# Kernel optimization log

Measured on AMD Instinct MI355X. Metric: run time of the kernel, lower is better.

## Reference

```python
import jax, jax.numpy as jnp
import numpy as np

H = 14
N = H * H
DIM = 768
INT = 5
LAM = 3.5


def fft_conv_grouped(x, w):
    # x: (B, g*in_c, N) real; w: (g, int_c, in_c, H, H//2+1) complex
    g, int_c, in_c = w.shape[:3]
    B = x.shape[0]
    xf = jnp.fft.rfftn(x.reshape(B, g, in_c, H, H), axes=(-2, -1), norm='ortho')
    yf = jnp.einsum('bgchf,gichf->bgihf', xf, w)
    y = jnp.fft.irfftn(yf, s=(H, H), axes=(-2, -1), norm='ortho')
    return y.reshape(B, g * int_c, N)


def soft(x, t):
    # sign(x) * relu(|x| - t)
    return jnp.sign(x) * jnp.maximum(jnp.abs(x) - t, 0.0)


def batch_norm(x, gamma, beta, eps=1e-5):
    # training-mode BatchNorm1d applied per channel over (B, N); x: (B, N, C)
    m = x.mean(axis=(0, 1))
    v = x.var(axis=(0, 1))
    return (x - m) * jax.lax.rsqrt(v + eps) * gamma + beta


def setup_inputs() -> dict:
    key = jax.random.key(0)
    ks = jax.random.split(key, 8)
    B = 32
    Hf = H // 2 + 1
    # kernel: init randn*0.06, then normalize_parameters()
    kr = jax.random.normal(ks[0], (DIM, INT, 1, H, Hf, 2), dtype=jnp.float32) * 0.06
    kc = kr[..., 0] + 1j * kr[..., 1]
    nrm = jnp.sqrt((jnp.abs(kc) ** 2).sum(axis=(2, 3, 4), keepdims=True) * 2.0 / H ** 2)
    kc = kc / nrm
    kernel = jnp.stack([jnp.real(kc), jnp.imag(kc)], axis=-1)
    # L buffer: update_L(lam=1) -> per-group max singular value of Gram kk
    kk = jnp.einsum('gichf,gjchf->gijhf', kc, jnp.conj(kc))
    sv = np.linalg.svd(np.asarray(jnp.transpose(kk, (0, 3, 4, 1, 2))), compute_uv=False)
    L = jnp.asarray(sv.reshape(DIM, -1).max(axis=-1), dtype=jnp.float32)
    hid = 4 * DIM
    return {
        'x': jax.random.normal(ks[1], (B, N, DIM), dtype=jnp.float32),
        'v_w': jax.random.normal(ks[2], (DIM, DIM), dtype=jnp.float32) * 0.02,
        'proj_w': jax.random.normal(ks[3], (DIM, DIM), dtype=jnp.float32) * 0.02,
        'proj_b': jnp.zeros((DIM,), dtype=jnp.float32),
        'kernel': kernel,
        'kernel2': jax.random.normal(ks[4], (DIM, 1, 1, H, Hf, 2), dtype=jnp.float32) * 0.02,
        'n1_g': jnp.ones((DIM,), dtype=jnp.float32),
        'n1_b': jnp.zeros((DIM,), dtype=jnp.float32),
        'n2_g': jnp.ones((DIM,), dtype=jnp.float32),
        'n2_b': jnp.zeros((DIM,), dtype=jnp.float32),
        'fc1_w': jax.random.normal(ks[5], (hid, DIM), dtype=jnp.float32) * 0.02,
        'fc1_b': jnp.zeros((hid,), dtype=jnp.float32),
        'fc2_w': jax.random.normal(ks[6], (DIM, hid), dtype=jnp.float32) * 0.02,
        'fc2_b': jnp.zeros((DIM,), dtype=jnp.float32),
        'L': L,
    }


def reference(x, v_w, proj_w, proj_b, kernel, kernel2, n1_g, n1_b, n2_g, n2_b, fc1_w, fc1_b, fc2_w, fc2_b, L):
    k = kernel[..., 0] + 1j * kernel[..., 1]                 # (g, int, 1, H, Hf)
    kk = jnp.einsum('gichf,gjchf->gijhf', k, jnp.conj(k))     # (g, int, int, H, Hf)
    vx = x @ v_w.T                                            # v Linear, no bias
    xc = jnp.swapaxes(vx, -2, -1)                             # (B, C, N)
    u = fft_conv_grouped(xc, k)                               # (B, g*int, N)
    Lv = jnp.repeat(L, INT)[None, :, None]                    # (1, g*int, 1)
    # ISTA: init soft-threshold then 3 gradient + shrink steps
    s = soft(u, LAM)
    for _ in range(3):
        s = s - (fft_conv_grouped(s, kk) - u) / Lv
        s = soft(s, LAM / Lv)
    # reconstruct with conjugate-transposed kernel, then mix with kernel2
    new = fft_conv_grouped(s, jnp.swapaxes(jnp.conj(k), 1, 2))  # (B, g, N)
    k2 = kernel2[..., 0] + 1j * kernel2[..., 1]
    new = fft_conv_grouped(new, k2)
    new = jnp.swapaxes(new, -2, -1)                           # (B, N, C)
    new = x + (batch_norm(new, n1_g, n1_b) @ proj_w.T + proj_b)
    h = jax.nn.gelu(batch_norm(new, n2_g, n2_b) @ fc1_w.T + fc1_b, approximate=False)
    return new + (h @ fc2_w.T + fc2_b)
```

## Files before the change

### kernel.cpp

```cpp
#include <hip/hip_runtime.h>
#include <cmath>

typedef unsigned short u16;
typedef __bf16 bf16x8 __attribute__((ext_vector_type(8)));
typedef float f32x4 __attribute__((ext_vector_type(4)));
typedef float float4v __attribute__((ext_vector_type(4)));
typedef u16 ushort4v __attribute__((ext_vector_type(4)));
typedef u16 ushort8v __attribute__((ext_vector_type(8)));

#define DIMC 768
#define NP 196
#define MTOT 6272
#define HIDC 3072
#define LAMC 3.5f

__device__ const float C14d[14] = {
  1.0f, 0.9009688679024191f, 0.6234898018587336f, 0.22252093395631445f,
  -0.22252093395631445f, -0.6234898018587336f, -0.9009688679024191f, -1.0f,
  -0.9009688679024191f, -0.6234898018587336f, -0.22252093395631445f,
  0.22252093395631445f, 0.6234898018587336f, 0.9009688679024191f
};
__device__ const float S14d[14] = {
  0.0f, 0.43388373911755823f, 0.7818314824680298f, 0.9749279121818236f,
  0.9749279121818236f, 0.7818314824680298f, 0.43388373911755823f, 0.0f,
  -0.43388373911755823f, -0.7818314824680298f, -0.9749279121818236f,
  -0.9749279121818236f, -0.7818314824680298f, -0.43388373911755823f
};

__device__ __forceinline__ u16 f2bf(float f) {
  unsigned u = __builtin_bit_cast(unsigned, f);
  unsigned r = u + 0x7FFFu + ((u >> 16) & 1u);
  return (u16)(r >> 16);
}

__device__ __forceinline__ size_t fidx(int m, int k, int K) {
  return ((size_t)(m >> 4) * (K >> 5) + (k >> 5)) * 512 +
         (size_t)((((k >> 3) & 3) * 16 + (m & 15)) * 8 + (k & 7));
}

__global__ __launch_bounds__(256) void prep_k(
    const float* __restrict__ v_w, const float* __restrict__ fc2w,
    const float* __restrict__ x,
    u16* __restrict__ vwf, u16* __restrict__ fc2f, u16* __restrict__ xf,
    u16* __restrict__ Ff, u16* __restrict__ Gf) {
  const int bid = blockIdx.x, t = threadIdx.x;
  if (bid < 378) {
    int idx = bid * 256 + t;
    if (idx < 50176) {
      int j = idx & 7, lane = (idx >> 3) & 63;
      int mk = idx >> 9, k0 = mk % 7, m0 = mk / 7;
      int s = m0 * 16 + (lane & 15);
      int q = k0 * 32 + (lane >> 4) * 8 + j;
      float v = 0.f;
      if (q < 196) {
        int kr = s >> 4, f = (s >> 1) & 7, r = q / 14, c = q % 14;
        int th = (kr * r + f * c) % 14;
        v = (s & 1) ? -S14d[th] : C14d[th];
      }
      Ff[idx] = f2bf(v);
    } else {
      int t2 = idx - 50176;
      int j = t2 & 7, lane = (t2 >> 3) & 63;
      int pk = t2 >> 9, k0 = pk % 7, p0 = pk / 7;
      int p = p0 * 16 + (lane & 15);
      int s = k0 * 32 + (lane >> 4) * 8 + j;
      float v = 0.f;
      if (p < 196) {
        int kr = s >> 4, f = (s >> 1) & 7, r = p / 14, c = p % 14;
        int th = (kr * r + f * c) % 14;
        float w = (f == 0 || f == 7) ? 1.f : 2.f;
        v = (w * (1.f / 196.f)) * ((s & 1) ? -S14d[th] : C14d[th]);
      }
      Gf[t2] = f2bf(v);
    }
    return;
  }
  const float* src; u16* dst; int idx, K;
  if (bid < 666)        { src = v_w;  dst = vwf;  idx = (bid - 378) * 256 + t;  K = DIMC; }
  else if (bid < 1818)  { src = fc2w; dst = fc2f; idx = (bid - 666) * 256 + t;  K = HIDC; }
  else                  { src = x;    dst = xf;   idx = (bid - 1818) * 256 + t; K = DIMC; }
  const int KC = K >> 5;
  int chunk = idx >> 6, l = idx & 63;
  int row = (chunk / KC) * 16 + (l & 15);
  int k0 = (chunk % KC) * 32 + (l >> 4) * 8;
  const float* sp = src + (size_t)row * K + k0;
  float4v f0 = *(const float4v*)sp;
  float4v f1 = *(const float4v*)(sp + 4);
  ushort8v o;
#pragma unroll
  for (int j = 0; j < 4; ++j) { o[j] = f2bf(f0[j]); o[j + 4] = f2bf(f1[j]); }
  *(ushort8v*)(dst + (size_t)idx * 8) = o;
}

template<int EPI>
__global__ __launch_bounds__(256) void gemmw_k(
    const u16* __restrict__ Af, const u16* __restrict__ Bf,
    const float* __restrict__ bias, const float* __restrict__ res,
    void* __restrict__ Cp, int Nr, int Kr, int NB) {
  const int t = threadIdx.x, w = t >> 6, lane = t & 63;
  const int bid = blockIdx.x;
  const int xcd = bid & 7, j = bid >> 3;
  const int mt = xcd + 8 * (j / NB);
  if (mt >= 98) return;
  const int m0 = mt * 64;
  const int n0 = ((j % NB) * 4 + w) * 64;
  const int KC = Kr >> 5;
  const int l15 = lane & 15, l4 = lane >> 4;

  const u16* Ab = Af + ((size_t)(m0 >> 4) * KC) * 512 + lane * 8;
  const u16* Bb = Bf + ((size_t)(n0 >> 4) * KC) * 512 + lane * 8;

  f32x4 acc[4][4];
#pragma unroll
  for (int a = 0; a < 4; ++a)
#pragma unroll
    for (int b2 = 0; b2 < 4; ++b2) acc[a][b2] = (f32x4){0.f, 0.f, 0.f, 0.f};

  for (int kc = 0; kc < KC; ++kc) {
    bf16x8 af[4], bfv[4];
#pragma unroll
    for (int mb = 0; mb < 4; ++mb)
      af[mb] = *(const bf16x8*)(Ab + ((size_t)mb * KC + kc) * 512);
#pragma unroll
    for (int nb = 0; nb < 4; ++nb)
      bfv[nb] = *(const bf16x8*)(Bb + ((size_t)nb * KC + kc) * 512);
#pragma unroll
    for (int mb = 0; mb < 4; ++mb)
#pragma unroll
      for (int nb = 0; nb < 4; ++nb)
        acc[mb][nb] = __builtin_amdgcn_mfma_f32_16x16x32_bf16(af[mb], bfv[nb], acc[mb][nb], 0, 0, 0);
  }

#pragma unroll
  for (int mb = 0; mb < 4; ++mb) {
#pragma unroll
    for (int nb = 0; nb < 4; ++nb) {
      int n = n0 + nb * 16 + l15;
      if (EPI == 0) {
        int m0r = m0 + mb * 16 + l4 * 4;
        int bb = m0r / 196, np0 = m0r - bb * 196;
        *(float4v*)&((float*)Cp)[((size_t)bb * DIMC + n) * 196 + np0] =
            (float4v){acc[mb][nb][0], acc[mb][nb][1], acc[mb][nb][2], acc[mb][nb][3]};
      } else {
#pragma unroll
        for (int r = 0; r < 4; ++r) {
          int m = m0 + mb * 16 + l4 * 4 + r;
          float v = acc[mb][nb][r];
          if (EPI == 1) {
            ((float*)Cp)[(size_t)m * Nr + n] = v + bias[n] + res[(size_t)m * Nr + n];
          } else {
            float vb = v + bias[n];
            float ge = 0.5f * vb * (1.f + erff(vb * 0.70710678118654752f));
            ((u16*)Cp)[fidx(m, n, Nr)] = f2bf(ge);
          }
        }
      }
    }
  }
}

__global__ __launch_bounds__(64) void checkmfma_k(
    const float* __restrict__ vxt, const float* __restrict__ kern,
    const u16* __restrict__ Ff, const u16* __restrict__ Gf,
    int* __restrict__ cnt, int* __restrict__ wl) {
  __shared__ float xf[16 * 228];
  const int lane = threadIdx.x;
  const int wgb = blockIdx.x;
  const int g = wgb >> 1, bhalf = wgb & 1;
  const int tl = lane & 15, h = lane >> 4;
  const float* xbase = vxt + ((size_t)(bhalf * 16 + tl) * DIMC + g) * 196;

  bf16x8 Bx[7];
#pragma unroll
  for (int k0 = 0; k0 < 7; ++k0) {
    int q0 = k0 * 32 + h * 8;
    ushort8v tv;
    if (k0 < 6) {
      float4v f0 = *(const float4v*)(xbase + q0);
      float4v f1 = *(const float4v*)(xbase + q0 + 4);
#pragma unroll
      for (int j = 0; j < 4; ++j) { tv[j] = f2bf(f0[j]); tv[j + 4] = f2bf(f1[j]); }
    } else {
#pragma unroll
      for (int j = 0; j < 8; ++j) {
        int q = q0 + j;
        tv[j] = (q < 196) ? f2bf(xbase[q]) : (u16)0;
      }
    }
    Bx[k0] = __builtin_bit_cast(bf16x8, tv);
  }

  for (int m0 = 0; m0 < 14; ++m0) {
    f32x4 acc = (f32x4){0.f, 0.f, 0.f, 0.f};
#pragma unroll
    for (int k0 = 0; k0 < 7; ++k0) {
      bf16x8 Af = __builtin_bit_cast(bf16x8,
          *(const ushort8v*)(Ff + ((size_t)(m0 * 7 + k0) * 64 + lane) * 8));
      acc = __builtin_amdgcn_mfma_f32_16x16x32_bf16(Af, Bx[k0], acc, 0, 0, 0);
    }
    *(f32x4*)&xf[tl * 228 + m0 * 16 + h * 4] = acc;
  }

  bf16x8 By[5][7];
#pragma unroll
  for (int i = 0; i < 5; ++i) {
    const float* kb = kern + ((size_t)g * 5 + i) * 224;
#pragma unroll
    for (int k0 = 0; k0 < 7; ++k0) {
      f32x4 x0 = *(const f32x4*)&xf[tl * 228 + k0 * 32 + h * 8];
      f32x4 x1 = *(const f32x4*)&xf[tl * 228 + k0 * 32 + h * 8 + 4];
      int mb = k0 * 16 + h * 4;
      float2 ka = *(const float2*)(kb + (mb + 0) * 2);
      float2 kc = *(const float2*)(kb + (mb + 1) * 2);
      float2 ke = *(const float2*)(kb + (mb + 2) * 2);
      float2 kg = *(const float2*)(kb + (mb + 3) * 2);
      ushort8v tv;
      tv[0] = f2bf(ka.x * x0[0] - ka.y * x0[1]);
      tv[1] = f2bf(ka.x * x0[1] + ka.y * x0[0]);
      tv[2] = f2bf(kc.x * x0[2] - kc.y * x0[3]);
      tv[3] = f2bf(kc.x * x0[3] + kc.y * x0[2]);
      tv[4] = f2bf(ke.x * x1[0] - ke.y * x1[1]);
      tv[5] = f2bf(ke.x * x1[1] + ke.y * x1[0]);
      tv[6] = f2bf(kg.x * x1[2] - kg.y * x1[3]);
      tv[7] = f2bf(kg.x * x1[3] + kg.y * x1[2]);
      By[i][k0] = __builtin_bit_cast(bf16x8, tv);
    }
  }

  float vmax = 0.f;
  for (int p0 = 0; p0 < 13; ++p0) {
    f32x4 a0 = (f32x4){0.f, 0.f, 0.f, 0.f};
    f32x4 a1 = a0, a2 = a0, a3 = a0, a4 = a0;
#pragma unroll
    for (int k0 = 0; k0 < 7; ++k0) {
      bf16x8 Ag = __builtin_bit_cast(bf16x8,
          *(const ushort8v*)(Gf + ((size_t)(p0 * 7 + k0) * 64 + lane) * 8));
      a0 = __builtin_amdgcn_mfma_f32_16x16x32_bf16(Ag, By[0][k0], a0, 0, 0, 0);
      a1 = __builtin_amdgcn_mfma_f32_16x16x32_bf16(Ag, By[1][k0], a1, 0, 0, 0);
      a2 = __builtin_amdgcn_mfma_f32_16x16x32_bf16(Ag, By[2][k0], a2, 0, 0, 0);
      a3 = __builtin_amdgcn_mfma_f32_16x16x32_bf16(Ag, By[3][k0], a3, 0, 0, 0);
      a4 = __builtin_amdgcn_mfma_f32_16x16x32_bf16(Ag, By[4][k0], a4, 0, 0, 0);
    }
#pragma unroll
    for (int r = 0; r < 4; ++r) {
      vmax = fmaxf(vmax, fabsf(a0[r]));
      vmax = fmaxf(vmax, fabsf(a1[r]));
      vmax = fmaxf(vmax, fabsf(a2[r]));
      vmax = fmaxf(vmax, fabsf(a3[r]));
      vmax = fmaxf(vmax, fabsf(a4[r]));
    }
  }
  vmax = fmaxf(vmax, __shfl_xor(vmax, 16));
  vmax = fmaxf(vmax, __shfl_xor(vmax, 32));
  if (lane < 16 && vmax > (LAMC - 0.1f)) {
    int idx = atomicAdd(cnt, 1);
    wl[idx] = g * 32 + bhalf * 16 + lane;
  }
}

__global__ __launch_bounds__(64) void slow_k(
    const float* __restrict__ vxt, const float* __restrict__ kern,
    const float* __restrict__ kern2, const float* __restrict__ Lbuf,
    const int* __restrict__ cnt, const int* __restrict__ wl,
    float* __restrict__ outp,
    float* __restrict__ tsum, float* __restrict__ tsq,
    unsigned* __restrict__ maskg, unsigned* __restrict__ bmask) {
  const int ntile = *cnt;
  if ((int)blockIdx.x >= ntile) return;
  const int t = threadIdx.x;
  __shared__ float TC[196], TSn[196];
  __shared__ float xs[196];
  __shared__ float t1R[112], t1I[112];
  __shared__ float t2R[112], t2I[112];
  __shared__ float zr[112], zi[112];
  __shared__ float kR[5][112], kI[5][112];
  __shared__ float uu[5][196];
  __shared__ float ss[5][196];
  __shared__ float k2R[112], k2I[112];

  for (int i = t; i < 196; i += 64) {
    int a = i / 14, c = i - (i / 14) * 14;
    int m = (a * c) % 14;
    TC[i] = C14d[m]; TSn[i] = S14d[m];
  }

  auto rowsFwd = [&](const float* xsrc) {
    for (int i = t; i < 112; i += 64) {
      int r = i >> 3, f = i & 7;
      const float* xp = xsrc + r * 14;
      const float* tc = &TC[f * 14]; const float* tsn = &TSn[f * 14];
      float ar = 0.f, ai = 0.f;
#pragma unroll
      for (int c = 0; c < 14; ++c) { float xv = xp[c]; ar += xv * tc[c]; ai -= xv * tsn[c]; }
      t1R[i] = ar; t1I[i] = ai;
    }
    __syncthreads();
  };
  auto colsFwd = [&](float* oR, float* oI) {
    for (int i = t; i < 112; i += 64) {
      int kr = i >> 3, f = i & 7;
      const float* tc = &TC[kr * 14]; const float* tsn = &TSn[kr * 14];
      float br = 0.f, bi = 0.f;
#pragma unroll
      for (int r = 0; r < 14; ++r) {
        float xr = t1R[r * 8 + f], xi = t1I[r * 8 + f];
        br += tc[r] * xr + tsn[r] * xi;
        bi += tc[r] * xi - tsn[r] * xr;
      }
      oR[i] = br; oI[i] = bi;
    }
    __syncthreads();
  };
  auto colsInv = [&]() {
    for (int i = t; i < 112; i += 64) {
      int r = i >> 3, f = i & 7;
      const float* tc = &TC[r * 14]; const float* tsn = &TSn[r * 14];
      float br = 0.f, bi = 0.f;
#pragma unroll
      for (int kr = 0; kr < 14; ++kr) {
        float xr = t1R[kr * 8 + f], xi = t1I[kr * 8 + f];
        br += tc[kr] * xr - tsn[kr] * xi;
        bi += tc[kr] * xi + tsn[kr] * xr;
      }
      t2R[i] = br; t2I[i] = bi;
    }
    __syncthreads();
  };
  auto rowVal = [&](int r, int c) -> float {
    const float* pR = &t2R[r * 8]; const float* pI = &t2I[r * 8];
    float v = pR[0] + ((c & 1) ? -pR[7] : pR[7]);
    float s2 = 0.f;
#pragma unroll
    for (int f = 1; f < 7; ++f) s2 += pR[f] * TC[f * 14 + c] - pI[f] * TSn[f * 14 + c];
    return (v + 2.f * s2) * (1.0f / 196.0f);
  };

  for (int widx = blockIdx.x; widx < ntile; widx += gridDim.x) {
    const int tile = wl[widx];
    const int g = tile >> 5, b = tile & 31;
    __syncthreads();
    for (int i = t; i < 560; i += 64) {
      int ii = i / 112, p = i - ii * 112;
      const float* kp = kern + ((size_t)g * 5 + ii) * 224 + p * 2;
      kR[ii][p] = kp[0]; kI[ii][p] = kp[1];
    }
    for (int i = t; i < 196; i += 64) xs[i] = vxt[((size_t)b * DIMC + g) * 196 + i];
    for (int i = t; i < 112; i += 64) {
      k2R[i] = kern2[(size_t)g * 224 + i * 2];
      k2I[i] = kern2[(size_t)g * 224 + i * 2 + 1];
    }
    __syncthreads();

    rowsFwd(xs);
    colsFwd(zr, zi);
    for (int ii = 0; ii < 5; ++ii) {
      for (int i = t; i < 112; i += 64) {
        float a = kR[ii][i], b2 = kI[ii][i];
        t1R[i] = a * zr[i] - b2 * zi[i];
        t1I[i] = a * zi[i] + b2 * zr[i];
      }
      __syncthreads();
      colsInv();
      for (int i = t; i < 196; i += 64) uu[ii][i] = rowVal(i / 14, i - (i / 14) * 14);
      __syncthreads();
    }

    const float invL = 1.0f / Lbuf[g];
    const float thr = LAMC * invL;
    {
      float* up = &uu[0][0];
      float* sp = &ss[0][0];
      for (int i = t; i < 980; i += 64) {
        float v = up[i];
        float a = fabsf(v) - LAMC;
        sp[i] = a > 0.f ? copysignf(a, v) : 0.f;
      }
    }
    __syncthreads();

    for (int iter = 0; iter < 4; ++iter) {
      for (int i = t; i < 112; i += 64) { zr[i] = 0.f; zi[i] = 0.f; }
      __syncthreads();
      for (int ii = 0; ii < 5; ++ii) {
        rowsFwd(&ss[ii][0]);
        colsFwd(t2R, t2I);
        for (int i = t; i < 112; i += 64) {
          float a = kR[ii][i], b2 = kI[ii][i];
          zr[i] += a * t2R[i] + b2 * t2I[i];
          zi[i] += a * t2I[i] - b2 * t2R[i];
        }
        __syncthreads();
      }
      if (iter == 3) break;
      for (int ii = 0; ii < 5; ++ii) {
        for (int i = t; i < 112; i += 64) {
          float a = kR[ii][i], b2 = kI[ii][i];
          t1R[i] = a * zr[i] - b2 * zi[i];
          t1I[i] = a * zi[i] + b2 * zr[i];
        }
        __syncthreads();
        colsInv();
        for (int i = t; i < 196; i += 64) {
          float v = rowVal(i / 14, i - (i / 14) * 14);
          float sv = ss[ii][i] - (v - uu[ii][i]) * invL;
          float aa = fabsf(sv) - thr;
          ss[ii][i] = aa > 0.f ? copysignf(aa, sv) : 0.f;
        }
        __syncthreads();
      }
    }

    if (t < 28) {
      int kr = t >> 1, f = (t & 1) * 7;
      int d = kr * 8 + f;
      int srci = ((14 - kr) % 14) * 8 + f;
      float pr = 0.5f * (zr[d] + zr[srci]);
      float pi = 0.5f * (zi[d] - zi[srci]);
      zr[d] = pr; zi[d] = pi;
    }
    __syncthreads();
    for (int i = t; i < 112; i += 64) {
      float a = k2R[i], b2 = k2I[i];
      t1R[i] = a * zr[i] - b2 * zi[i];
      t1I[i] = a * zi[i] + b2 * zr[i];
    }
    __syncthreads();
    colsInv();
    float sacc = 0.f, qacc = 0.f;
    for (int i = t; i < 196; i += 64) {
      float v = rowVal(i / 14, i - (i / 14) * 14);
      outp[((size_t)(b * 196 + i)) * DIMC + g] = v;
      sacc += v; qacc += v * v;
    }
#pragma unroll
    for (int off = 32; off; off >>= 1) {
      sacc += __shfl_xor(sacc, off);
      qacc += __shfl_xor(qacc, off);
    }
    if (t == 0) {
      tsum[tile] = sacc; tsq[tile] = qacc;
      atomicOr(&maskg[g], 1u << b);
      atomicOr(bmask, 1u << b);
    }
  }
}

__global__ __launch_bounds__(256) void stats1c0_k(
    const float* __restrict__ tsum, const float* __restrict__ tsq,
    const unsigned* __restrict__ maskg,
    const float* __restrict__ gam, const float* __restrict__ bet,
    const float* __restrict__ projw, const float* __restrict__ pb,
    float* __restrict__ sc1, float* __restrict__ c0) {
  __shared__ float sh1s[768];
  const int t = threadIdx.x;
  for (int c = t; c < DIMC; c += 256) {
    unsigned mask = maskg[c];
    float S = 0.f, Q = 0.f;
    if (mask) {
      for (int b = 0; b < 32; ++b)
        if ((mask >> b) & 1) { S += tsum[c * 32 + b]; Q += tsq[c * 32 + b]; }
    }
    float m = S * (1.0f / 6272.0f);
    float v = fmaxf(Q * (1.0f / 6272.0f) - m * m, 0.f);
    float rs = rsqrtf(v + 1e-5f);
    float sc = gam[c] * rs;
    sh1s[c] = bet[c] - m * sc;
    if (blockIdx.x == 0) sc1[c] = sc;
  }
  __syncthreads();
  int n = blockIdx.x * 256 + t;
  const float* row = projw + (size_t)n * DIMC;
  float s = 0.f;
  for (int g = 0; g < DIMC; g += 4) {
    float4v r = *(const float4v*)(row + g);
    s += r[0] * sh1s[g] + r[1] * sh1s[g + 1] + r[2] * sh1s[g + 2] + r[3] * sh1s[g + 3];
  }
  c0[n] = s + pb[n];
}

__global__ __launch_bounds__(256) void bnb_k(
    const float* __restrict__ x, const float* __restrict__ c0,
    const float* __restrict__ sc1, const unsigned* __restrict__ maskg,
    const unsigned* __restrict__ bmask, const float* __restrict__ newm,
    const float* __restrict__ projw,
    float* __restrict__ new2, u16* __restrict__ n2f,
    float* __restrict__ part) {
  const int jb = blockIdx.x, b = blockIdx.y, t = threadIdx.x;
  __shared__ unsigned gm[24];
  __shared__ float c0s[768];
  const bool hasb = ((*bmask >> b) & 1u) != 0u;
  if (t < 24) {
    unsigned w = 0;
    if (hasb)
      for (int j2 = 0; j2 < 32; ++j2) w |= ((maskg[t * 32 + j2] >> b) & 1u) << j2;
    gm[t] = w;
  }
  for (int c = t; c < 768; c += 256) c0s[c] = c0[c];
  __syncthreads();

  float S0 = 0, S1 = 0, S2 = 0, Q0 = 0, Q1 = 0, Q2 = 0;
  for (int mr = 0; mr < 7; ++mr) {
    int m = b * 196 + jb * 7 + mr;
    size_t row = (size_t)m * DIMC;
#pragma unroll
    for (int j2 = 0; j2 < 3; ++j2) {
      int n = t + j2 * 256;
      float v = x[row + n] + c0s[n];
      if (hasb) {
        for (int w = 0; w < 24; ++w) {
          unsigned bits = gm[w];
          while (bits) {
            int g = w * 32 + __builtin_ctz(bits);
            bits &= bits - 1;
            v += sc1[g] * newm[row + g] * projw[(size_t)n * DIMC + g];
          }
        }
      }
      new2[row + n] = v;
      n2f[fidx(m, n, DIMC)] = f2bf(v);
      if (j2 == 0) { S0 += v; Q0 += v * v; }
      else if (j2 == 1) { S1 += v; Q1 += v * v; }
      else { S2 += v; Q2 += v * v; }
    }
  }
  float* p = part + (size_t)(b * 28 + jb) * 1536;
  p[t] = S0; p[t + 256] = S1; p[t + 512] = S2;
  p[768 + t] = Q0; p[768 + 256 + t] = Q1; p[768 + 512 + t] = Q2;
}

__global__ __launch_bounds__(256) void red2_k(const float* __restrict__ part,
                                              float* __restrict__ part2) {
  int slot = blockIdx.x * 256 + threadIdx.x;
  int b = blockIdx.y;
  float s = 0.f;
  const float* p = part + (size_t)(b * 28) * 1536 + slot;
  for (int jb = 0; jb < 28; ++jb) s += p[(size_t)jb * 1536];
  part2[(size_t)b * 1536 + slot] = s;
}

__global__ __launch_bounds__(256) void stats2fin_k(const float* __restrict__ part2,
    const float* __restrict__ gam, const float* __restrict__ bet,
    float* __restrict__ scale, float* __restrict__ shift) {
  int c = blockIdx.x * 256 + threadIdx.x;
  float S = 0.f, Q = 0.f;
  for (int b = 0; b < 32; ++b) {
    S += part2[(size_t)b * 1536 + c];
    Q += part2[(size_t)b * 1536 + 768 + c];
  }
  float m = S * (1.0f / 6272.0f);
  float v = fmaxf(Q * (1.0f / 6272.0f) - m * m, 0.f);
  float rs = rsqrtf(v + 1e-5f);
  float sc = gam[c] * rs;
  scale[c] = sc;
  shift[c] = bet[c] - m * sc;
}

__global__ __launch_bounds__(256) void foldfc1_k(const float* __restrict__ fc1w,
    const float* __restrict__ fc1b, const float* __restrict__ sc2,
    const float* __restrict__ sh2, u16* __restrict__ fc1s,
    float* __restrict__ d0) {
  const int bid = blockIdx.x, t = threadIdx.x;
  if (bid < 12) {
    int n = bid * 256 + t;
    const float* row = fc1w + (size_t)n * DIMC;
    float s = 0.f;
    for (int k = 0; k < DIMC; k += 4) {
      float4v r = *(const float4v*)(row + k);
      float4v h = *(const float4v*)(sh2 + k);
      s += r[0] * h[0] + r[1] * h[1] + r[2] * h[2] + r[3] * h[3];
    }
    d0[n] = s + fc1b[n];
  } else {
    int idx = (bid - 12) * 256 + t;
    int chunk = idx >> 6, l = idx & 63;
    int n = (chunk / 24) * 16 + (l & 15);
    int k0 = (chunk % 24) * 32 + (l >> 4) * 8;
    const float* sp = fc1w + (size_t)n * DIMC + k0;
    float4v f0 = *(const float4v*)sp;
    float4v f1 = *(const float4v*)(sp + 4);
    float4v s0 = *(const float4v*)(sc2 + k0);
    float4v s1 = *(const float4v*)(sc2 + k0 + 4);
    f0 = f0 * s0; f1 = f1 * s1;
    ushort8v o;
#pragma unroll
    for (int j = 0; j < 4; ++j) { o[j] = f2bf(f0[j]); o[j + 4] = f2bf(f1[j]); }
    *(ushort8v*)(fc1s + (size_t)idx * 8) = o;
  }
}

extern "C" void kernel_launch(void* const* d_in, const int* in_sizes, int n_in,
                              void* d_out, int out_size, void* d_ws, size_t ws_size,
                              hipStream_t stream) {
  (void)in_sizes; (void)n_in; (void)out_size;
  const float* x      = (const float*)d_in[0];
  const float* v_w    = (const float*)d_in[1];
  const float* proj_w = (const float*)d_in[2];
  const float* proj_b = (const float*)d_in[3];
  const float* kern   = (const float*)d_in[4];
  const float* kern2  = (const float*)d_in[5];
  const float* n1g    = (const float*)d_in[6];
  const float* n1b    = (const float*)d_in[7];
  const float* n2g    = (const float*)d_in[8];
  const float* n2b    = (const float*)d_in[9];
  const float* fc1w   = (const float*)d_in[10];
  const float* fc1b   = (const float*)d_in[11];
  const float* fc2w   = (const float*)d_in[12];
  const float* fc2b   = (const float*)d_in[13];
  const float* Lb     = (const float*)d_in[14];
  float* out = (float*)d_out;

  char* ws = (char*)d_ws;
  size_t o = 0;
  auto alloc = [&](size_t bytes) { size_t r = o; o += (bytes + 255) & ~(size_t)255; return r; };
  u16*   vwf    = (u16*)(ws + alloc(589824 * 2));
  u16*   fc2f   = (u16*)(ws + alloc(2359296 * 2));
  u16*   fc1s   = (u16*)(ws + alloc(2359296 * 2));
  u16*   Ffb    = (u16*)(ws + alloc(50176 * 2));
  u16*   Gfb    = (u16*)(ws + alloc(46592 * 2));
  float* sc1    = (float*)(ws + alloc(768 * 4));
  float* sc2    = (float*)(ws + alloc(768 * 4));
  float* sh2    = (float*)(ws + alloc(768 * 4));
  float* c0     = (float*)(ws + alloc(768 * 4));
  float* d0     = (float*)(ws + alloc(3072 * 4));
  float* part   = (float*)(ws + alloc((size_t)896 * 1536 * 4));
  float* part2  = (float*)(ws + alloc((size_t)32 * 1536 * 4));
  char*  zblk   = (char*)(ws + alloc(4096));
  int*      cnt   = (int*)zblk;
  unsigned* bmask = (unsigned*)(zblk + 4);
  unsigned* maskg = (unsigned*)(zblk + 8);
  int*   wl     = (int*)(ws + alloc(24576 * 4));
  float* tsum   = (float*)(ws + alloc(24576 * 4));
  float* tsq    = (float*)(ws + alloc(24576 * 4));
  u16*   xf     = (u16*)(ws + alloc((size_t)MTOT * DIMC * 2));
  u16*   n2f    = (u16*)(ws + alloc((size_t)MTOT * DIMC * 2));
  float* vxt    = (float*)(ws + alloc((size_t)MTOT * DIMC * 4));
  float* newm   = (float*)(ws + alloc((size_t)MTOT * DIMC * 4));
  float* new2   = (float*)(ws + alloc((size_t)MTOT * DIMC * 4));
  u16*   hbf    = (u16*)vxt;
  if (ws_size < o) return;

  hipMemsetAsync(zblk, 0, 4096, stream);

  prep_k<<<4170, 256, 0, stream>>>(v_w, fc2w, x, vwf, fc2f, xf, Ffb, Gfb);
  gemmw_k<0><<<312, 256, 0, stream>>>(xf, vwf, nullptr, nullptr, vxt, DIMC, DIMC, 3);
  checkmfma_k<<<1536, 64, 0, stream>>>(vxt, kern, Ffb, Gfb, cnt, wl);
  slow_k<<<1024, 64, 0, stream>>>(vxt, kern, kern2, Lb, cnt, wl, newm,
                                  tsum, tsq, maskg, bmask);
  stats1c0_k<<<3, 256, 0, stream>>>(tsum, tsq, maskg, n1g, n1b, proj_w, proj_b, sc1, c0);
  bnb_k<<<dim3(28, 32), 256, 0, stream>>>(x, c0, sc1, maskg, bmask, newm, proj_w,
                                          new2, n2f, part);
  red2_k<<<dim3(6, 32), 256, 0, stream>>>(part, part2);
  stats2fin_k<<<3, 256, 0, stream>>>(part2, n2g, n2b, sc2, sh2);
  foldfc1_k<<<1164, 256, 0, stream>>>(fc1w, fc1b, sc2, sh2, fc1s, d0);
  gemmw_k<2><<<1248, 256, 0, stream>>>(n2f, fc1s, d0, nullptr, hbf, HIDC, DIMC, 12);
  gemmw_k<1><<<312, 256, 0, stream>>>(hbf, fc2f, fc2b, new2, out, DIMC, HIDC, 3);
}
```

Before: 273.4 us.

## Double-buffer GEMM register loads and split sparsity check across two blocks

The bf16 MFMA GEMM now prefetches the next K-chunk of A/B fragments into a second register set while issuing MFMAs on the current one. It also raises wave priority around the MFMA bursts and adds an occupancy hint to launch_bounds, all to hide global load latency. The sparsity screening kernel splits the 5 interior channels across two blocks (3+2), doubling the grid to raise parallelism and cut per-block registers. The worklist buffer is doubled to match. The catch is that both halves can enqueue the same tile, so slow_k may see duplicate entries.

```diff
diff --git a/kernel.cpp b/kernel.cpp
--- a/kernel.cpp
+++ b/kernel.cpp
@@ -93,7 +93,7 @@
 }
 
 template<int EPI>
-__global__ __launch_bounds__(256) void gemmw_k(
+__global__ __launch_bounds__(256, 3) void gemmw_k(
     const u16* __restrict__ Af, const u16* __restrict__ Bf,
     const float* __restrict__ bias, const float* __restrict__ res,
     void* __restrict__ Cp, int Nr, int Kr, int NB) {
@@ -116,19 +116,41 @@
 #pragma unroll
     for (int b2 = 0; b2 < 4; ++b2) acc[a][b2] = (f32x4){0.f, 0.f, 0.f, 0.f};
 
-  for (int kc = 0; kc < KC; ++kc) {
-    bf16x8 af[4], bfv[4];
+  bf16x8 a0[4], b0[4], a1[4], b1[4];
+#pragma unroll
+  for (int mb = 0; mb < 4; ++mb) a0[mb] = *(const bf16x8*)(Ab + ((size_t)mb * KC) * 512);
+#pragma unroll
+  for (int nb = 0; nb < 4; ++nb) b0[nb] = *(const bf16x8*)(Bb + ((size_t)nb * KC) * 512);
+
+  for (int kc = 0; kc < KC; kc += 2) {
 #pragma unroll
     for (int mb = 0; mb < 4; ++mb)
-      af[mb] = *(const bf16x8*)(Ab + ((size_t)mb * KC + kc) * 512);
+      a1[mb] = *(const bf16x8*)(Ab + ((size_t)mb * KC + kc + 1) * 512);
 #pragma unroll
     for (int nb = 0; nb < 4; ++nb)
-      bfv[nb] = *(const bf16x8*)(Bb + ((size_t)nb * KC + kc) * 512);
+      b1[nb] = *(const bf16x8*)(Bb + ((size_t)nb * KC + kc + 1) * 512);
+    __builtin_amdgcn_s_setprio(1);
 #pragma unroll
     for (int mb = 0; mb < 4; ++mb)
 #pragma unroll
       for (int nb = 0; nb < 4; ++nb)
-        acc[mb][nb] = __builtin_amdgcn_mfma_f32_16x16x32_bf16(af[mb], bfv[nb], acc[mb][nb], 0, 0, 0);
+        acc[mb][nb] = __builtin_amdgcn_mfma_f32_16x16x32_bf16(a0[mb], b0[nb], acc[mb][nb], 0, 0, 0);
+    __builtin_amdgcn_s_setprio(0);
+    if (kc + 2 < KC) {
+#pragma unroll
+      for (int mb = 0; mb < 4; ++mb)
+        a0[mb] = *(const bf16x8*)(Ab + ((size_t)mb * KC + kc + 2) * 512);
+#pragma unroll
+      for (int nb = 0; nb < 4; ++nb)
+        b0[nb] = *(const bf16x8*)(Bb + ((size_t)nb * KC + kc + 2) * 512);
+    }
+    __builtin_amdgcn_s_setprio(1);
+#pragma unroll
+    for (int mb = 0; mb < 4; ++mb)
+#pragma unroll
+      for (int nb = 0; nb < 4; ++nb)
+        acc[mb][nb] = __builtin_amdgcn_mfma_f32_16x16x32_bf16(a1[mb], b1[nb], acc[mb][nb], 0, 0, 0);
+    __builtin_amdgcn_s_setprio(0);
   }
 
 #pragma unroll
@@ -166,7 +188,8 @@
   __shared__ float xf[16 * 228];
   const int lane = threadIdx.x;
   const int wgb = blockIdx.x;
-  const int g = wgb >> 1, bhalf = wgb & 1;
+  const int g = wgb >> 2, bhalf = (wgb >> 1) & 1, ihalf = wgb & 1;
+  const int i0 = ihalf ? 3 : 0, ni = ihalf ? 2 : 3;
   const int tl = lane & 15, h = lane >> 4;
   const float* xbase = vxt + ((size_t)(bhalf * 16 + tl) * DIMC + g) * 196;
 
@@ -201,53 +224,52 @@
     *(f32x4*)&xf[tl * 228 + m0 * 16 + h * 4] = acc;
   }
 
-  bf16x8 By[5][7];
-#pragma unroll
-  for (int i = 0; i < 5; ++i) {
-    const float* kb = kern + ((size_t)g * 5 + i) * 224;
-#pragma unroll
-    for (int k0 = 0; k0 < 7; ++k0) {
-      f32x4 x0 = *(const f32x4*)&xf[tl * 228 + k0 * 32 + h * 8];
-      f32x4 x1 = *(const f32x4*)&xf[tl * 228 + k0 * 32 + h * 8 + 4];
-      int mb = k0 * 16 + h * 4;
-      float2 ka = *(const float2*)(kb + (mb + 0) * 2);
-      float2 kc = *(const float2*)(kb + (mb + 1) * 2);
-      float2 ke = *(const float2*)(kb + (mb + 2) * 2);
-      float2 kg = *(const float2*)(kb + (mb + 3) * 2);
-      ushort8v tv;
-      tv[0] = f2bf(ka.x * x0[0] - ka.y * x0[1]);
-      tv[1] = f2bf(ka.x * x0[1] + ka.y * x0[0]);
-      tv[2] = f2bf(kc.x * x0[2] - kc.y * x0[3]);
-      tv[3] = f2bf(kc.x * x0[3] + kc.y * x0[2]);
-      tv[4] = f2bf(ke.x * x1[0] - ke.y * x1[1]);
-      tv[5] = f2bf(ke.x * x1[1] + ke.y * x1[0]);
-      tv[6] = f2bf(kg.x * x1[2] - kg.y * x1[3]);
-      tv[7] = f2bf(kg.x * x1[3] + kg.y * x1[2]);
-      By[i][k0] = __builtin_bit_cast(bf16x8, tv);
+  bf16x8 By[3][7];
+#pragma unroll
+  for (int ii = 0; ii < 3; ++ii) {
+    if (ii < ni) {
+      const float* kb = kern + ((size_t)g * 5 + i0 + ii) * 224;
+#pragma unroll
+      for (int k0 = 0; k0 < 7; ++k0) {
+        f32x4 x0 = *(const f32x4*)&xf[tl * 228 + k0 * 32 + h * 8];
+        f32x4 x1 = *(const f32x4*)&xf[tl * 228 + k0 * 32 + h * 8 + 4];
+        int mb = k0 * 16 + h * 4;
+        float2 ka = *(const float2*)(kb + (mb + 0) * 2);
+        float2 kc = *(const float2*)(kb + (mb + 1) * 2);
+        float2 ke = *(const float2*)(kb + (mb + 2) * 2);
+        float2 kg = *(const float2*)(kb + (mb + 3) * 2);
+        ushort8v tv;
+        tv[0] = f2bf(ka.x * x0[0] - ka.y * x0[1]);
+        tv[1] = f2bf(ka.x * x0[1] + ka.y * x0[0]);
+        tv[2] = f2bf(kc.x * x0[2] - kc.y * x0[3]);
+        tv[3] = f2bf(kc.x * x0[3] + kc.y * x0[2]);
+        tv[4] = f2bf(ke.x * x1[0] - ke.y * x1[1]);
+        tv[5] = f2bf(ke.x * x1[1] + ke.y * x1[0]);
+        tv[6] = f2bf(kg.x * x1[2] - kg.y * x1[3]);
+        tv[7] = f2bf(kg.x * x1[3] + kg.y * x1[2]);
+        By[ii][k0] = __builtin_bit_cast(bf16x8, tv);
+      }
     }
   }
 
   float vmax = 0.f;
   for (int p0 = 0; p0 < 13; ++p0) {
     f32x4 a0 = (f32x4){0.f, 0.f, 0.f, 0.f};
-    f32x4 a1 = a0, a2 = a0, a3 = a0, a4 = a0;
+    f32x4 a1 = a0, a2 = a0;
 #pragma unroll
     for (int k0 = 0; k0 < 7; ++k0) {
       bf16x8 Ag = __builtin_bit_cast(bf16x8,
           *(const ushort8v*)(Gf + ((size_t)(p0 * 7 + k0) * 64 + lane) * 8));
       a0 = __builtin_amdgcn_mfma_f32_16x16x32_bf16(Ag, By[0][k0], a0, 0, 0, 0);
       a1 = __builtin_amdgcn_mfma_f32_16x16x32_bf16(Ag, By[1][k0], a1, 0, 0, 0);
-      a2 = __builtin_amdgcn_mfma_f32_16x16x32_bf16(Ag, By[2][k0], a2, 0, 0, 0);
-      a3 = __builtin_amdgcn_mfma_f32_16x16x32_bf16(Ag, By[3][k0], a3, 0, 0, 0);
-      a4 = __builtin_amdgcn_mfma_f32_16x16x32_bf16(Ag, By[4][k0], a4, 0, 0, 0);
+      if (ni == 3)
+        a2 = __builtin_amdgcn_mfma_f32_16x16x32_bf16(Ag, By[2][k0], a2, 0, 0, 0);
     }
 #pragma unroll
     for (int r = 0; r < 4; ++r) {
       vmax = fmaxf(vmax, fabsf(a0[r]));
       vmax = fmaxf(vmax, fabsf(a1[r]));
-      vmax = fmaxf(vmax, fabsf(a2[r]));
-      vmax = fmaxf(vmax, fabsf(a3[r]));
-      vmax = fmaxf(vmax, fabsf(a4[r]));
+      if (ni == 3) vmax = fmaxf(vmax, fabsf(a2[r]));
     }
   }
   vmax = fmaxf(vmax, __shfl_xor(vmax, 16));
@@ -628,7 +650,7 @@
   int*      cnt   = (int*)zblk;
   unsigned* bmask = (unsigned*)(zblk + 4);
   unsigned* maskg = (unsigned*)(zblk + 8);
-  int*   wl     = (int*)(ws + alloc(24576 * 4));
+  int*   wl     = (int*)(ws + alloc(49152 * 4));
   float* tsum   = (float*)(ws + alloc(24576 * 4));
   float* tsq    = (float*)(ws + alloc(24576 * 4));
   u16*   xf     = (u16*)(ws + alloc((size_t)MTOT * DIMC * 2));
@@ -643,7 +665,7 @@
 
   prep_k<<<4170, 256, 0, stream>>>(v_w, fc2w, x, vwf, fc2f, xf, Ffb, Gfb);
   gemmw_k<0><<<312, 256, 0, stream>>>(xf, vwf, nullptr, nullptr, vxt, DIMC, DIMC, 3);
-  checkmfma_k<<<1536, 64, 0, stream>>>(vxt, kern, Ffb, Gfb, cnt, wl);
+  checkmfma_k<<<3072, 64, 0, stream>>>(vxt, kern, Ffb, Gfb, cnt, wl);
   slow_k<<<1024, 64, 0, stream>>>(vxt, kern, kern2, Lb, cnt, wl, newm,
                                   tsum, tsq, maskg, bmask);
   stats1c0_k<<<3, 256, 0, stream>>>(tsum, tsq, maskg, n1g, n1b, proj_w, proj_b, sc1, c0);
```

New measurement: 294.4 us. 1.08x slower.
